# Kernel optimization log

Measured on AMD Instinct MI355X. Metric: run time of the kernel, lower is better.

## Reference

```python
import jax, jax.numpy as jnp
import numpy as np

T, B, D = 512, 128, 1024  # time, batch, feature == hidden_size


def setup_inputs() -> dict:
    key = jax.random.key(0)
    k0, k1, k2, k3 = jax.random.split(key, 4)
    scale = 1.0 / np.sqrt(D)
    ins = jax.random.normal(k0, (T, B, D), jnp.float32)
    resets = jax.random.randint(k1, (T, B), 0, 2).astype(bool)
    # flax GRUCell params, fused along gate axis in order (r, z, n)
    Wi = jax.random.normal(k2, (D, 3 * D), jnp.float32) * scale   # ir|iz|in (with bias)
    bi = jnp.zeros((3 * D,), jnp.float32)
    Wh = jax.random.normal(k3, (D, 3 * D), jnp.float32) * scale   # hr|hz|hn (hr,hz no bias)
    bhn = jnp.zeros((D,), jnp.float32)                            # bias only on hn branch
    return {"ins": ins, "resets": resets, "Wi": Wi, "bi": bi, "Wh": Wh, "bhn": bhn}


def reference(ins, resets, Wi, bi, Wh, bhn):
    H = Wh.shape[0]
    # Input projections are time-independent: compute once as a big GEMM.
    xi = jnp.einsum('tbd,dg->tbg', ins, Wi) + bi  # [T, B, 3H]

    def step(h, inp):
        xi_t, reset_t = inp                       # [B, 3H], [B]
        h = jnp.where(reset_t[:, None], jnp.zeros_like(h), h)  # reset carry to zeros
        hh = h @ Wh                               # [B, 3H]
        xr, xz, xn = jnp.split(xi_t, 3, axis=-1)
        hr, hz, hn = jnp.split(hh, 3, axis=-1)
        r = jax.nn.sigmoid(xr + hr)
        z = jax.nn.sigmoid(xz + hz)
        n = jnp.tanh(xn + r * (hn + bhn))
        h_new = (1.0 - z) * n + z * h             # flax GRUCell update
        return h_new, h_new                       # GRUCell returns (new_h, new_h)

    h0 = jnp.zeros((ins.shape[1], H), ins.dtype)
    _, ys = jax.lax.scan(step, h0, (xi, resets))
    return ys  # [T, B, H]
```

## Files before the change

### kernel.cpp

```cpp
#include <hip/hip_runtime.h>
#include <stdint.h>

typedef unsigned short u16;
typedef unsigned int u32;
typedef unsigned char u8;

typedef __attribute__((ext_vector_type(4))) float f32x4;
typedef __attribute__((ext_vector_type(2))) u32 u32x2;
typedef __attribute__((ext_vector_type(4))) u32 u32x4;
typedef __attribute__((ext_vector_type(8))) __bf16 bf16x8;

#define NITER 48
#define TT 512
#define BB 128

__device__ __forceinline__ u16 f2bf(float f){
    u32 u = __builtin_bit_cast(u32, f);
    u = (u + 0x7FFFu + ((u >> 16) & 1u)) >> 16;
    return (u16)u;
}
__device__ __forceinline__ float bf2f(u16 v){
    u32 u = ((u32)v) << 16;
    return __builtin_bit_cast(float, u);
}
__device__ __forceinline__ u32x4 pack8(f32x4 a, f32x4 b){
    u32x4 u;
    u[0] = (u32)f2bf(a[0]) | ((u32)f2bf(a[1]) << 16);
    u[1] = (u32)f2bf(a[2]) | ((u32)f2bf(a[3]) << 16);
    u[2] = (u32)f2bf(b[0]) | ((u32)f2bf(b[1]) << 16);
    u[3] = (u32)f2bf(b[2]) | ((u32)f2bf(b[3]) << 16);
    return u;
}
__device__ __forceinline__ void glds16(const u16* g, u16* l){
    __builtin_amdgcn_global_load_lds(
        (const __attribute__((address_space(1))) u32*)g,
        (__attribute__((address_space(3))) u32*)l, 16, 0, 0);
}

__global__ void k_detect(const u8* __restrict__ r, int* __restrict__ flag){
    __shared__ int nz[4];
    if (threadIdx.x < 4) nz[threadIdx.x] = 0;
    __syncthreads();
    int loc[4] = {0,0,0,0};
    const int base = threadIdx.x * 16;
    #pragma unroll
    for (int i = 0; i < 16; ++i) if (r[base + i]) loc[i & 3] = 1;
    #pragma unroll
    for (int j = 0; j < 4; ++j) if (loc[j]) atomicOr(&nz[j], 1);
    __syncthreads();
    if (threadIdx.x == 0){
        int f;
        if (nz[0] && !nz[1] && !nz[2] && !nz[3]) f = 0;
        else if (!nz[0] && !nz[1] && (nz[2] || nz[3])) f = 2;
        else f = 1;
        *flag = f;
    }
}

__device__ __forceinline__ int reset_at(const void* r, int f, int idx){
    if (f == 0) return ((const int*)r)[idx] != 0;
    if (f == 1) return ((const u8*)r)[idx] != 0;
    return ((const float*)r)[idx] != 0.f;
}

__global__ void k_ages(const void* __restrict__ resets, const int* __restrict__ flag,
                       int b0, int bw_log, u8* __restrict__ age, int* __restrict__ counts){
    __shared__ int lc[NITER];
    const int tid = threadIdx.x;
    if (tid < NITER) lc[tid] = 0;
    __syncthreads();
    const int cid = blockIdx.x * 256 + tid;
    const int f = *flag;
    const int bwm = (1 << bw_log) - 1;
    const int t = cid >> bw_log, b = b0 + (cid & bwm);
    int a = 0, tt = t;
    while (tt > 0 && !reset_at(resets, f, tt * BB + b)){ ++a; --tt; }
    if (a > NITER - 1) a = NITER - 1;
    age[cid] = (u8)a;
    atomicAdd(&lc[a], 1);
    __syncthreads();
    if (tid < NITER && lc[tid]) atomicAdd(&counts[tid], lc[tid]);
}

__global__ void k_offsets(const int* __restrict__ counts, int* __restrict__ offs,
                          int* __restrict__ curs){
    if (threadIdx.x == 0){
        int o = 0;
        for (int i = 0; i < NITER; ++i){ offs[i] = o; curs[i] = o; o += counts[i]; }
        offs[NITER] = o;
    }
}

__global__ void k_scatter(const u8* __restrict__ age, int* __restrict__ curs,
                          u16* __restrict__ list, u16* __restrict__ posof){
    __shared__ int lc[NITER], lb[NITER];
    const int tid = threadIdx.x;
    if (tid < NITER) lc[tid] = 0;
    __syncthreads();
    const int cid = blockIdx.x * 256 + tid;
    const int a = age[cid];
    const int lpos = atomicAdd(&lc[a], 1);
    __syncthreads();
    if (tid < NITER && lc[tid]) lb[tid] = atomicAdd(&curs[tid], lc[tid]);
    __syncthreads();
    const int p = lb[a] + lpos;
    list[p] = (u16)cid;
    posof[cid] = (u16)p;
}

__global__ void k_packT(const float* __restrict__ Wi, const float* __restrict__ Wh,
                        u16* __restrict__ Wit, u16* __restrict__ Wht){
    __shared__ float tl[32][33];
    const int kb = blockIdx.x * 32;
    const int nb = blockIdx.y * 32;
    const float* W = blockIdx.z ? Wh : Wi;
    u16* Wt = blockIdx.z ? Wht : Wit;
    const int tx = threadIdx.x;
    for (int r = threadIdx.y; r < 32; r += 8)
        tl[r][tx] = W[(size_t)(kb + r) * 3072 + nb + tx];
    __syncthreads();
    for (int r = threadIdx.y; r < 32; r += 8)
        Wt[(size_t)(nb + r) * 1024 + kb + tx] = f2bf(tl[tx][r]);
}

__global__ void k_tobf(const float* __restrict__ ins, u16* __restrict__ insbf,
                       int b0, int bw_log, int total8){
    const int bwm = (1 << bw_log) - 1;
    for (int i = blockIdx.x * 256 + threadIdx.x; i < total8; i += gridDim.x * 256){
        const int cid = i >> 7;
        const int c8 = (i & 127) * 8;
        const int t = cid >> bw_log, j = cid & bwm;
        const float* src = ins + (size_t)(t * BB + b0 + j) * 1024 + c8;
        f32x4 a = *(const f32x4*)src;
        f32x4 b = *(const f32x4*)(src + 4);
        *(u32x4*)(insbf + (size_t)cid * 1024 + c8) = pack8(a, b);
    }
}

__global__ __launch_bounds__(256, 4)
void k_xi(const u16* __restrict__ insbf, const u16* __restrict__ Wit,
          u16* __restrict__ xi, int Mrows)
{
    __shared__ __align__(16) u16 lds[2][8192];
    const int tid = threadIdx.x;
    const int lane = tid & 63;
    const int w = tid >> 6;
    const int wr = w >> 1, wc = w & 1;
    const int l15 = lane & 15;
    const int l4 = lane >> 4;

    const int nMt = Mrows >> 7;
    const int nTiles = nMt * 24;

    for (int idx = blockIdx.x; idx < nTiles; idx += gridDim.x){
        const int mt = idx / 24;
        const int cg = idx - mt * 24;
        const int m0 = mt * 128;
        const int c0 = cg * 128;

        const u16* ga0 = insbf + (size_t)(m0 + w * 16 + (lane >> 2)) * 1024 + (lane & 3) * 8;
        const u16* ga1 = ga0 + (size_t)64 * 1024;
        const u16* gb0 = Wit + (size_t)(c0 + w * 16 + (lane >> 2)) * 1024 + (lane & 3) * 8;
        const u16* gb1 = gb0 + (size_t)64 * 1024;

        f32x4 acc[4][4];
        #pragma unroll
        for (int i = 0; i < 4; ++i)
            #pragma unroll
            for (int j = 0; j < 4; ++j)
                acc[i][j] = (f32x4){0.f, 0.f, 0.f, 0.f};

        {
            u16* Lb = lds[0];
            glds16(ga0, &Lb[w * 512]);
            glds16(ga1, &Lb[2048 + w * 512]);
            glds16(gb0, &Lb[4096 + w * 512]);
            glds16(gb1, &Lb[6144 + w * 512]);
        }
        __syncthreads();

        for (int kt = 0; kt < 32; ++kt){
            if (kt < 31){
                u16* Nb = lds[(kt + 1) & 1];
                const int ko = (kt + 1) * 32;
                glds16(ga0 + ko, &Nb[w * 512]);
                glds16(ga1 + ko, &Nb[2048 + w * 512]);
                glds16(gb0 + ko, &Nb[4096 + w * 512]);
                glds16(gb1 + ko, &Nb[6144 + w * 512]);
            }
            const u16* L = lds[kt & 1];
            bf16x8 ax[4], bx[4];
            #pragma unroll
            for (int rf = 0; rf < 4; ++rf)
                ax[rf] = *(const bf16x8*)&L[(wr * 64 + rf * 16 + l15) * 32 + l4 * 8];
            #pragma unroll
            for (int cf = 0; cf < 4; ++cf)
                bx[cf] = *(const bf16x8*)&L[4096 + (wc * 64 + cf * 16 + l15) * 32 + l4 * 8];
            #pragma unroll
            for (int cf = 0; cf < 4; ++cf)
                #pragma unroll
                for (int rf = 0; rf < 4; ++rf)
                    acc[cf][rf] = __builtin_amdgcn_mfma_f32_16x16x32_bf16(
                        bx[cf], ax[rf], acc[cf][rf], 0, 0, 0);
            __syncthreads();
        }

        #pragma unroll
        for (int cf = 0; cf < 4; ++cf){
            #pragma unroll
            for (int rf = 0; rf < 4; ++rf){
                const int R = m0 + wr * 64 + rf * 16 + l15;
                const int N0 = c0 + wc * 64 + cf * 16 + l4 * 4;
                u32x2 v;
                v[0] = (u32)f2bf(acc[cf][rf][0]) | ((u32)f2bf(acc[cf][rf][1]) << 16);
                v[1] = (u32)f2bf(acc[cf][rf][2]) | ((u32)f2bf(acc[cf][rf][3]) << 16);
                *(u32x2*)(xi + (size_t)R * 3072 + N0) = v;
            }
        }
    }
}

__global__ void k_h0(const u16* __restrict__ list, const int* __restrict__ counts,
                     const u16* __restrict__ xi, float* __restrict__ ys,
                     u16* __restrict__ hbf,
                     const float* __restrict__ bi, const float* __restrict__ bhn,
                     int b0, int bw_log)
{
    const int total = counts[0] * 128;
    const int bwm = (1 << bw_log) - 1;
    for (int i = blockIdx.x * 256 + threadIdx.x; i < total; i += gridDim.x * 256){
        const int row = i >> 7;
        const int c8 = (i & 127) * 8;
        const int cid = list[row];
        const int p = ((cid >> bw_log) << 7) + b0 + (cid & bwm);
        const u16* xr = xi + (size_t)cid * 3072 + c8;
        u32x4 vr = *(const u32x4*)xr;
        u32x4 vz = *(const u32x4*)(xr + 1024);
        u32x4 vn = *(const u32x4*)(xr + 2048);
        f32x4 br0 = *(const f32x4*)(bi + c8),        br1 = *(const f32x4*)(bi + c8 + 4);
        f32x4 bz0 = *(const f32x4*)(bi + 1024 + c8), bz1 = *(const f32x4*)(bi + 1024 + c8 + 4);
        f32x4 bn0 = *(const f32x4*)(bi + 2048 + c8), bn1 = *(const f32x4*)(bi + 2048 + c8 + 4);
        f32x4 bh0 = *(const f32x4*)(bhn + c8),       bh1 = *(const f32x4*)(bhn + c8 + 4);
        float out[8];
        #pragma unroll
        for (int e = 0; e < 8; ++e){
            const float xrv = bf2f((u16)(vr[e >> 1] >> ((e & 1) * 16)));
            const float xzv = bf2f((u16)(vz[e >> 1] >> ((e & 1) * 16)));
            const float xnv = bf2f((u16)(vn[e >> 1] >> ((e & 1) * 16)));
            const float brv = (e < 4) ? br0[e] : br1[e - 4];
            const float bzv = (e < 4) ? bz0[e] : bz1[e - 4];
            const float bnv = (e < 4) ? bn0[e] : bn1[e - 4];
            const float bhv = (e < 4) ? bh0[e] : bh1[e - 4];
            const float rr = 1.f / (1.f + __expf(-(xrv + brv)));
            const float zz = 1.f / (1.f + __expf(-(xzv + bzv)));
            const float nn = tanhf(xnv + bnv + rr * bhv);
            out[e] = (1.f - zz) * nn;
        }
        float* dst = ys + (size_t)p * 1024 + c8;
        f32x4 o0 = (f32x4){out[0], out[1], out[2], out[3]};
        f32x4 o1 = (f32x4){out[4], out[5], out[6], out[7]};
        *(f32x4*)dst = o0;
        *(f32x4*)(dst + 4) = o1;
        *(u32x4*)(hbf + (size_t)row * 1024 + c8) = pack8(o0, o1);
    }
}

#define SSTR64 64
#define SAB 0
#define SBB 8192
#define SLB64 20480
__global__ __launch_bounds__(256, 2)
void k_scanh(int iter, const u16* __restrict__ list, const int* __restrict__ offs,
             const int* __restrict__ counts, const u16* __restrict__ posof,
             u16* hbf, const u16* __restrict__ xi,
             float* ys, const u16* __restrict__ Wht,
             const float* __restrict__ bi, const float* __restrict__ bhn,
             int b0, int bw_log)
{
    const int count = counts[iter];
    if (count <= 0) return;
    const int off = offs[iter];
    const int nTiles = ((count + 127) >> 7) * 16;
    const int bwm = (1 << bw_log) - 1;
    const int bwv = 1 << bw_log;

    __shared__ __align__(16) u16 lds[2][SLB64];

    const int tid = threadIdx.x;
    const int lane = tid & 63;
    const int w = tid >> 6;
    const int wr = w >> 1;
    const int wc = w & 1;
    const int l15 = lane & 15;
    const int l4 = lane >> 4;
    const int lrow = lane >> 3;
    const int slot = lane & 7;

    for (int tile = blockIdx.x; tile < nTiles; tile += gridDim.x){
        const int mt = tile >> 4;
        const int cg = tile & 15;
        const int m0 = mt * 128;
        const int c0 = cg * 64;

        const u16* pa[4];
        #pragma unroll
        for (int c = 0; c < 4; ++c){
            const int r = c * 32 + w * 8 + lrow;
            const int cid = list[off + min(m0 + r, count - 1)];
            pa[c] = hbf + (size_t)posof[cid - bwv] * 1024 + slot * 8;
        }
        const u16* pw[6];
        #pragma unroll
        for (int c = 0; c < 6; ++c){
            const int br = c * 32 + w * 8 + lrow;
            const int g = br >> 6, ri = br & 63;
            pw[c] = Wht + (size_t)(g * 1024 + c0 + ri) * 1024 + slot * 8;
        }

        f32x4 acc[3][4][2];
        #pragma unroll
        for (int gi = 0; gi < 3; ++gi)
            #pragma unroll
            for (int rf = 0; rf < 4; ++rf)
                #pragma unroll
                for (int cf = 0; cf < 2; ++cf)
                    acc[gi][rf][cf] = (f32x4){0.f, 0.f, 0.f, 0.f};

        {
            u16* N = lds[0];
            #pragma unroll
            for (int c = 0; c < 4; ++c)
                glds16(pa[c], &N[SAB + (c * 32 + w * 8) * SSTR64]);
            #pragma unroll
            for (int c = 0; c < 6; ++c)
                glds16(pw[c], &N[SBB + (c * 32 + w * 8) * SSTR64]);
        }
        __syncthreads();

        for (int kt = 0; kt < 16; ++kt){
            if (kt < 15){
                u16* N = lds[(kt + 1) & 1];
                const int ko = (kt + 1) * 64;
                #pragma unroll
                for (int c = 0; c < 4; ++c)
                    glds16(pa[c] + ko, &N[SAB + (c * 32 + w * 8) * SSTR64]);
                #pragma unroll
                for (int c = 0; c < 6; ++c)
                    glds16(pw[c] + ko, &N[SBB + (c * 32 + w * 8) * SSTR64]);
            }
            const u16* L = lds[kt & 1];
            #pragma unroll
            for (int kk = 0; kk < 2; ++kk){
                bf16x8 ah[4];
                #pragma unroll
                for (int rf = 0; rf < 4; ++rf)
                    ah[rf] = *(const bf16x8*)&L[SAB + (wr * 64 + rf * 16 + l15) * SSTR64 + kk * 32 + l4 * 8];
                #pragma unroll
                for (int g = 0; g < 3; ++g){
                    #pragma unroll
                    for (int cf = 0; cf < 2; ++cf){
                        bf16x8 bh = *(const bf16x8*)&L[SBB + (g * 64 + wc * 32 + cf * 16 + l15) * SSTR64 + kk * 32 + l4 * 8];
                        #pragma unroll
                        for (int rf = 0; rf < 4; ++rf)
                            acc[g][rf][cf] = __builtin_amdgcn_mfma_f32_16x16x32_bf16(
                                ah[rf], bh, acc[g][rf][cf], 0, 0, 0);
                    }
                }
            }
            __syncthreads();
        }

        #pragma unroll
        for (int cf = 0; cf < 2; ++cf){
            const int colh = c0 + wc * 32 + cf * 16 + l15;
            const float b_r = bi[colh];
            const float b_z = bi[1024 + colh];
            const float b_n = bi[2048 + colh];
            const float b_h = bhn[colh];
            #pragma unroll
            for (int rf = 0; rf < 4; ++rf){
                #pragma unroll
                for (int m = 0; m < 4; ++m){
                    const int rloc = wr * 64 + rf * 16 + l4 * 4 + m;
                    const int P = off + min(m0 + rloc, count - 1);
                    const int cid = list[P];
                    const int p = ((cid >> bw_log) << 7) + b0 + (cid & bwm);
                    const u16* xr = xi + (size_t)cid * 3072 + colh;
                    const float rr = 1.f / (1.f + __expf(-(bf2f(xr[0]) + b_r + acc[0][rf][cf][m])));
                    const float zz = 1.f / (1.f + __expf(-(bf2f(xr[1024]) + b_z + acc[1][rf][cf][m])));
                    const float nn = tanhf(bf2f(xr[2048]) + b_n + rr * (acc[2][rf][cf][m] + b_h));
                    const float hp = ys[(size_t)(p - 128) * 1024 + colh];
                    const float hv = (1.f - zz) * nn + zz * hp;
                    ys[(size_t)p * 1024 + colh] = hv;
                    hbf[(size_t)P * 1024 + colh] = f2bf(hv);
                }
            }
        }
    }
}

__global__ __launch_bounds__(256, 2)
void k_scan_fb(int iter, const u16* __restrict__ list, const int* __restrict__ offs,
               const int* __restrict__ counts, const float* __restrict__ ins,
               float* ys, const u16* __restrict__ Wit, const u16* __restrict__ Wht,
               const float* __restrict__ bi, const float* __restrict__ bhn)
{
    const int count = counts[iter];
    if (count <= 0) return;
    const int off = offs[iter];
    const int nTiles = ((count + 127) >> 7) * 16;
    const bool hasH = (iter > 0);

    __shared__ __align__(16) u16 lds[2][20480];

    const int tid = threadIdx.x;
    const int lane = tid & 63;
    const int w = tid >> 6;
    const int wr = w >> 1;
    const int wc = w & 1;
    const int l15 = lane & 15;
    const int l4 = lane >> 4;
    const int swz = ((l4 ^ (lane & 3)) * 8);
    const int sr = tid >> 2;
    const int sq = tid & 3;
    const int swzW = ((sq ^ (sr & 3)) * 8);

    for (int tile = blockIdx.x; tile < nTiles; tile += gridDim.x){
        const int mt = tile >> 4;
        const int cg = tile & 15;
        const int m0 = mt * 128;
        const int c0 = cg * 64;

        const int px0i = list[off + min(m0 + sr, count - 1)];
        const int px1i = list[off + min(m0 + 64 + sr, count - 1)];
        const float* px0 = ins + (size_t)px0i * 1024 + sq * 8;
        const float* px1 = ins + (size_t)px1i * 1024 + sq * 8;
        const float* ph0 = ys + (ptrdiff_t)(px0i - 128) * 1024 + sq * 8;
        const float* ph1 = ys + (ptrdiff_t)(px1i - 128) * 1024 + sq * 8;
        const u16* pb[6];
        #pragma unroll
        for (int pp = 0; pp < 6; ++pp){
            const int g = pp >> 1, m = pp & 1;
            const u16* W = m ? Wht : Wit;
            pb[pp] = W + (size_t)(g * 1024 + c0 + sr) * 1024 + sq * 8;
        }

        f32x4 acc[4][4][2];
        #pragma unroll
        for (int gi = 0; gi < 4; ++gi)
            #pragma unroll
            for (int rf = 0; rf < 4; ++rf)
                #pragma unroll
                for (int cf = 0; cf < 2; ++cf)
                    acc[gi][rf][cf] = (f32x4){0.f, 0.f, 0.f, 0.f};

        {
            u16* N = lds[0];
            *(u32x4*)&N[sr * 32 + swzW] = pack8(*(const f32x4*)(px0), *(const f32x4*)(px0 + 4));
            *(u32x4*)&N[(64 + sr) * 32 + swzW] = pack8(*(const f32x4*)(px1), *(const f32x4*)(px1 + 4));
            if (hasH){
                *(u32x4*)&N[(128 + sr) * 32 + swzW] = pack8(*(const f32x4*)(ph0), *(const f32x4*)(ph0 + 4));
                *(u32x4*)&N[(192 + sr) * 32 + swzW] = pack8(*(const f32x4*)(ph1), *(const f32x4*)(ph1 + 4));
            }
            #pragma unroll
            for (int pp = 0; pp < 6; ++pp)
                *(u32x4*)&N[8192 + (pp * 64 + sr) * 32 + swzW] = *(const u32x4*)(pb[pp]);
        }
        __syncthreads();

        int cur = 0;
        #pragma unroll 2
        for (int kt = 0; kt < 32; ++kt){
            f32x4 nx0a, nx0b, nx1a, nx1b, nh0a, nh0b, nh1a, nh1b;
            u32x4 sb[6];
            const bool more = (kt < 31);
            if (more){
                const int kof = (kt + 1) * 32;
                nx0a = *(const f32x4*)(px0 + kof); nx0b = *(const f32x4*)(px0 + kof + 4);
                nx1a = *(const f32x4*)(px1 + kof); nx1b = *(const f32x4*)(px1 + kof + 4);
                if (hasH){
                    nh0a = *(const f32x4*)(ph0 + kof); nh0b = *(const f32x4*)(ph0 + kof + 4);
                    nh1a = *(const f32x4*)(ph1 + kof); nh1b = *(const f32x4*)(ph1 + kof + 4);
                }
                #pragma unroll
                for (int pp = 0; pp < 6; ++pp) sb[pp] = *(const u32x4*)(pb[pp] + kof);
            }

            const u16* L = lds[cur];
            bf16x8 ax[4], ah[4];
            #pragma unroll
            for (int rf = 0; rf < 4; ++rf)
                ax[rf] = *(const bf16x8*)&L[(wr * 64 + rf * 16 + l15) * 32 + swz];
            if (hasH){
                #pragma unroll
                for (int rf = 0; rf < 4; ++rf)
                    ah[rf] = *(const bf16x8*)&L[(128 + wr * 64 + rf * 16 + l15) * 32 + swz];
            }
            #pragma unroll
            for (int g = 0; g < 3; ++g){
                #pragma unroll
                for (int cf = 0; cf < 2; ++cf){
                    const int brow = g * 128 + wc * 32 + cf * 16 + l15;
                    bf16x8 bv = *(const bf16x8*)&L[8192 + brow * 32 + swz];
                    const int gx = (g == 2) ? 2 : g;
                    #pragma unroll
                    for (int rf = 0; rf < 4; ++rf)
                        acc[gx][rf][cf] = __builtin_amdgcn_mfma_f32_16x16x32_bf16(
                            ax[rf], bv, acc[gx][rf][cf], 0, 0, 0);
                    if (hasH){
                        bf16x8 bh = *(const bf16x8*)&L[8192 + (brow + 64) * 32 + swz];
                        const int gh = (g == 2) ? 3 : g;
                        #pragma unroll
                        for (int rf = 0; rf < 4; ++rf)
                            acc[gh][rf][cf] = __builtin_amdgcn_mfma_f32_16x16x32_bf16(
                                ah[rf], bh, acc[gh][rf][cf], 0, 0, 0);
                    }
                }
            }

            if (more){
                u16* N = lds[cur ^ 1];
                *(u32x4*)&N[sr * 32 + swzW] = pack8(nx0a, nx0b);
                *(u32x4*)&N[(64 + sr) * 32 + swzW] = pack8(nx1a, nx1b);
                if (hasH){
                    *(u32x4*)&N[(128 + sr) * 32 + swzW] = pack8(nh0a, nh0b);
                    *(u32x4*)&N[(192 + sr) * 32 + swzW] = pack8(nh1a, nh1b);
                }
                #pragma unroll
                for (int pp = 0; pp < 6; ++pp)
                    *(u32x4*)&N[8192 + (pp * 64 + sr) * 32 + swzW] = sb[pp];
            }
            __syncthreads();
            cur ^= 1;
        }

        #pragma unroll
        for (int cf = 0; cf < 2; ++cf){
            const int colh = c0 + wc * 32 + cf * 16 + l15;
            const float b_r = bi[colh];
            const float b_z = bi[1024 + colh];
            const float b_n = bi[2048 + colh];
            const float b_h = bhn[colh];
            #pragma unroll
            for (int rf = 0; rf < 4; ++rf){
                #pragma unroll
                for (int m = 0; m < 4; ++m){
                    const int rloc = wr * 64 + rf * 16 + l4 * 4 + m;
                    const int p = list[off + min(m0 + rloc, count - 1)];
                    const float rr = 1.f / (1.f + __expf(-(acc[0][rf][cf][m] + b_r)));
                    const float zz = 1.f / (1.f + __expf(-(acc[1][rf][cf][m] + b_z)));
                    const float nn = tanhf(acc[2][rf][cf][m] + b_n + rr * (acc[3][rf][cf][m] + b_h));
                    float hp = 0.f;
                    if (hasH) hp = ys[(size_t)(p - 128) * 1024 + colh];
                    ys[(size_t)p * 1024 + colh] = (1.f - zz) * nn + zz * hp;
                }
            }
        }
    }
}

extern "C" void kernel_launch(void* const* d_in, const int* in_sizes, int n_in,
                              void* d_out, int out_size, void* d_ws, size_t ws_size,
                              hipStream_t stream)
{
    (void)in_sizes; (void)n_in; (void)out_size;
    const float* ins  = (const float*)d_in[0];
    const void*  rst  = d_in[1];
    const float* Wi   = (const float*)d_in[2];
    const float* bi   = (const float*)d_in[3];
    const float* Wh   = (const float*)d_in[4];
    const float* bhn  = (const float*)d_in[5];
    float* ys = (float*)d_out;
    u8* ws = (u8*)d_ws;

    u16* Wit    = (u16*)(ws + 0);
    u16* Wht    = (u16*)(ws + 6291456);
    u8*  age    = ws + 12582912;
    int* counts = (int*)(ws + 12648448);
    int* offs   = (int*)(ws + 12648704);
    int* curs   = (int*)(ws + 12648960);
    int* flag   = (int*)(ws + 12649216);
    u16* posof  = (u16*)(ws + 12649472);
    u16* list   = (u16*)(ws + 12780544);
    u16* insbf  = (u16*)(ws + 12911616);

    int bw = 0, bwlog = 0;
    {
        const size_t base = 12911616;
        if (ws_size >= base + (size_t)TT * 128 * 8192)      { bw = 128; bwlog = 7; }
        else if (ws_size >= base + (size_t)TT * 64 * 8192)  { bw = 64;  bwlog = 6; }
        else if (ws_size >= base + (size_t)TT * 32 * 8192)  { bw = 32;  bwlog = 5; }
    }

    k_detect<<<1, 256, 0, stream>>>((const u8*)rst, flag);
    k_packT<<<dim3(32, 96, 2), dim3(32, 8), 0, stream>>>(Wi, Wh, Wit, Wht);

    if (bw == 0){
        hipMemsetAsync(counts, 0, 192, stream);
        k_ages<<<TT * BB / 256, 256, 0, stream>>>(rst, flag, 0, 7, age, counts);
        k_offsets<<<1, 64, 0, stream>>>(counts, offs, curs);
        k_scatter<<<TT * BB / 256, 256, 0, stream>>>(age, curs, list, posof);
        for (int it = 0; it < NITER; ++it)
            k_scan_fb<<<512, 256, 0, stream>>>(it, list, offs, counts, ins, ys, Wit, Wht, bi, bhn);
        return;
    }

    u16* xi = insbf + (size_t)TT * bw * 1024;
    u16* hbf = insbf;
    const int nch = BB / bw;
    const int Mrows = TT * bw;

    for (int c = 0; c < nch; ++c){
        const int b0 = c * bw;
        hipMemsetAsync(counts, 0, 192, stream);
        k_ages<<<Mrows / 256, 256, 0, stream>>>(rst, flag, b0, bwlog, age, counts);
        k_offsets<<<1, 64, 0, stream>>>(counts, offs, curs);
        k_scatter<<<Mrows / 256, 256, 0, stream>>>(age, curs, list, posof);
        k_tobf<<<2048, 256, 0, stream>>>(ins, insbf, b0, bwlog, Mrows * 128);
        k_xi<<<3072, 256, 0, stream>>>(insbf, Wit, xi, Mrows);
        k_h0<<<2048, 256, 0, stream>>>(list, counts, xi, ys, hbf, bi, bhn, b0, bwlog);
        for (int it = 1; it < NITER; ++it){
            int est = ((Mrows >> (it + 1)) / 128 + 1) * 16;
            int grid = est < 32 ? 32 : (est > 512 ? 512 : est);
            k_scanh<<<grid, 256, 0, stream>>>(it, list, offs, counts, posof, hbf, xi,
                                              ys, Wht, bi, bhn, b0, bwlog);
        }
    }
}
```

Before: 1.997 ms.

## Fuse per-age scan launches into one persistent kernel with dataflow flags

Replaces the 47 per-age k_scanh launches and the separate k_h0 launch with a single persistent k_scan_all kernel. Tiles are ordered by age, and each one waits on per-group atomic completion counters for the previous age before it runs. The age sort becomes deterministic through per-block histograms and prefix bases instead of global atomics. The xi GEMM epilogue is staged through LDS so stores are coalesced 16-byte writes. This removes launch gaps and the tail idle time between dependent iterations, at the risk of spin-wait stalls or deadlock if dependent tiles are not resident.

```diff
diff --git a/kernel.cpp b/kernel.cpp
--- a/kernel.cpp
+++ b/kernel.cpp
@@ -6,7 +6,6 @@
 typedef unsigned char u8;
 
 typedef __attribute__((ext_vector_type(4))) float f32x4;
-typedef __attribute__((ext_vector_type(2))) u32 u32x2;
 typedef __attribute__((ext_vector_type(4))) u32 u32x4;
 typedef __attribute__((ext_vector_type(8))) __bf16 bf16x8;
 
@@ -64,7 +63,7 @@
 }
 
 __global__ void k_ages(const void* __restrict__ resets, const int* __restrict__ flag,
-                       int b0, int bw_log, u8* __restrict__ age, int* __restrict__ counts){
+                       int b0, int bw_log, u8* __restrict__ age, int* __restrict__ bh){
     __shared__ int lc[NITER];
     const int tid = threadIdx.x;
     if (tid < NITER) lc[tid] = 0;
@@ -79,33 +78,52 @@
     age[cid] = (u8)a;
     atomicAdd(&lc[a], 1);
     __syncthreads();
-    if (tid < NITER && lc[tid]) atomicAdd(&counts[tid], lc[tid]);
-}
-
-__global__ void k_offsets(const int* __restrict__ counts, int* __restrict__ offs,
-                          int* __restrict__ curs){
-    if (threadIdx.x == 0){
+    if (tid < NITER) bh[blockIdx.x * NITER + tid] = lc[tid];
+}
+
+__global__ void k_offsets(const int* __restrict__ bh, int NB,
+                          int* __restrict__ counts, int* __restrict__ offs,
+                          int* __restrict__ gbase, int* __restrict__ tbase,
+                          int* __restrict__ bb){
+    const int a = threadIdx.x;
+    if (a < NITER){
+        int run = 0;
+        for (int b = 0; b < NB; ++b){
+            bb[b * NITER + a] = run;
+            run += bh[b * NITER + a];
+        }
+        counts[a] = run;
+    }
+    __syncthreads();
+    if (a == 0){
         int o = 0;
-        for (int i = 0; i < NITER; ++i){ offs[i] = o; curs[i] = o; o += counts[i]; }
+        for (int i = 0; i < NITER; ++i){ offs[i] = o; o += counts[i]; }
         offs[NITER] = o;
-    }
-}
-
-__global__ void k_scatter(const u8* __restrict__ age, int* __restrict__ curs,
+        int g = 0, t = 0;
+        for (int i = 0; i < NITER; ++i){
+            const int ng = (counts[i] + 127) >> 7;
+            gbase[i] = g; g += ng;
+            tbase[i] = t; t += (i == 0) ? ng : ng * 16;
+        }
+        gbase[NITER] = g;
+        tbase[NITER] = t;
+    }
+}
+
+__global__ void k_scatter(const u8* __restrict__ age, const int* __restrict__ offs,
+                          const int* __restrict__ bb,
                           u16* __restrict__ list, u16* __restrict__ posof){
-    __shared__ int lc[NITER], lb[NITER];
+    __shared__ u8 sa[256];
     const int tid = threadIdx.x;
-    if (tid < NITER) lc[tid] = 0;
-    __syncthreads();
     const int cid = blockIdx.x * 256 + tid;
     const int a = age[cid];
-    const int lpos = atomicAdd(&lc[a], 1);
-    __syncthreads();
-    if (tid < NITER && lc[tid]) lb[tid] = atomicAdd(&curs[tid], lc[tid]);
-    __syncthreads();
-    const int p = lb[a] + lpos;
-    list[p] = (u16)cid;
-    posof[cid] = (u16)p;
+    sa[tid] = (u8)a;
+    __syncthreads();
+    int rank = 0;
+    for (int j = 0; j < tid; ++j) rank += (sa[j] == (u8)a);
+    const int pos = offs[a] + bb[blockIdx.x * NITER + a] + rank;
+    list[pos] = (u16)cid;
+    posof[cid] = (u16)pos;
 }
 
 __global__ void k_packT(const float* __restrict__ Wi, const float* __restrict__ Wh,
@@ -197,95 +215,84 @@
             for (int cf = 0; cf < 4; ++cf)
                 bx[cf] = *(const bf16x8*)&L[4096 + (wc * 64 + cf * 16 + l15) * 32 + l4 * 8];
             #pragma unroll
+            for (int rf = 0; rf < 4; ++rf)
+                #pragma unroll
+                for (int cf = 0; cf < 4; ++cf)
+                    acc[rf][cf] = __builtin_amdgcn_mfma_f32_16x16x32_bf16(
+                        ax[rf], bx[cf], acc[rf][cf], 0, 0, 0);
+            __syncthreads();
+        }
+
+        u16* region = ((u16*)lds) + w * 4096;
+        #pragma unroll
+        for (int rf = 0; rf < 4; ++rf)
+            #pragma unroll
             for (int cf = 0; cf < 4; ++cf)
                 #pragma unroll
-                for (int rf = 0; rf < 4; ++rf)
-                    acc[cf][rf] = __builtin_amdgcn_mfma_f32_16x16x32_bf16(
-                        bx[cf], ax[rf], acc[cf][rf], 0, 0, 0);
-            __syncthreads();
-        }
-
-        #pragma unroll
-        for (int cf = 0; cf < 4; ++cf){
-            #pragma unroll
-            for (int rf = 0; rf < 4; ++rf){
-                const int R = m0 + wr * 64 + rf * 16 + l15;
-                const int N0 = c0 + wc * 64 + cf * 16 + l4 * 4;
-                u32x2 v;
-                v[0] = (u32)f2bf(acc[cf][rf][0]) | ((u32)f2bf(acc[cf][rf][1]) << 16);
-                v[1] = (u32)f2bf(acc[cf][rf][2]) | ((u32)f2bf(acc[cf][rf][3]) << 16);
-                *(u32x2*)(xi + (size_t)R * 3072 + N0) = v;
-            }
-        }
-    }
-}
-
-__global__ void k_h0(const u16* __restrict__ list, const int* __restrict__ counts,
-                     const u16* __restrict__ xi, float* __restrict__ ys,
-                     u16* __restrict__ hbf,
-                     const float* __restrict__ bi, const float* __restrict__ bhn,
-                     int b0, int bw_log)
+                for (int m = 0; m < 4; ++m)
+                    region[(rf * 16 + l4 * 4 + m) * 64 + cf * 16 + l15] = f2bf(acc[rf][cf][m]);
+        #pragma unroll
+        for (int rep = 0; rep < 8; ++rep){
+            const int r = rep * 8 + (lane >> 3);
+            const int cc = (lane & 7) * 8;
+            u32x4 v = *(u32x4*)&region[r * 64 + cc];
+            *(u32x4*)(xi + (size_t)(m0 + wr * 64 + r) * 3072 + c0 + wc * 64 + cc) = v;
+        }
+        __syncthreads();
+    }
+}
+
+__device__ __forceinline__ void h0_body(int row, int c8, const u16* __restrict__ list,
+    const u16* __restrict__ xi, float* __restrict__ ys, u16* __restrict__ hbf,
+    const float* __restrict__ bi, const float* __restrict__ bhn, int b0, int bw_log)
 {
-    const int total = counts[0] * 128;
     const int bwm = (1 << bw_log) - 1;
-    for (int i = blockIdx.x * 256 + threadIdx.x; i < total; i += gridDim.x * 256){
-        const int row = i >> 7;
-        const int c8 = (i & 127) * 8;
-        const int cid = list[row];
-        const int p = ((cid >> bw_log) << 7) + b0 + (cid & bwm);
-        const u16* xr = xi + (size_t)cid * 3072 + c8;
-        u32x4 vr = *(const u32x4*)xr;
-        u32x4 vz = *(const u32x4*)(xr + 1024);
-        u32x4 vn = *(const u32x4*)(xr + 2048);
-        f32x4 br0 = *(const f32x4*)(bi + c8),        br1 = *(const f32x4*)(bi + c8 + 4);
-        f32x4 bz0 = *(const f32x4*)(bi + 1024 + c8), bz1 = *(const f32x4*)(bi + 1024 + c8 + 4);
-        f32x4 bn0 = *(const f32x4*)(bi + 2048 + c8), bn1 = *(const f32x4*)(bi + 2048 + c8 + 4);
-        f32x4 bh0 = *(const f32x4*)(bhn + c8),       bh1 = *(const f32x4*)(bhn + c8 + 4);
-        float out[8];
-        #pragma unroll
-        for (int e = 0; e < 8; ++e){
-            const float xrv = bf2f((u16)(vr[e >> 1] >> ((e & 1) * 16)));
-            const float xzv = bf2f((u16)(vz[e >> 1] >> ((e & 1) * 16)));
-            const float xnv = bf2f((u16)(vn[e >> 1] >> ((e & 1) * 16)));
-            const float brv = (e < 4) ? br0[e] : br1[e - 4];
-            const float bzv = (e < 4) ? bz0[e] : bz1[e - 4];
-            const float bnv = (e < 4) ? bn0[e] : bn1[e - 4];
-            const float bhv = (e < 4) ? bh0[e] : bh1[e - 4];
-            const float rr = 1.f / (1.f + __expf(-(xrv + brv)));
-            const float zz = 1.f / (1.f + __expf(-(xzv + bzv)));
-            const float nn = tanhf(xnv + bnv + rr * bhv);
-            out[e] = (1.f - zz) * nn;
-        }
-        float* dst = ys + (size_t)p * 1024 + c8;
-        f32x4 o0 = (f32x4){out[0], out[1], out[2], out[3]};
-        f32x4 o1 = (f32x4){out[4], out[5], out[6], out[7]};
-        *(f32x4*)dst = o0;
-        *(f32x4*)(dst + 4) = o1;
-        *(u32x4*)(hbf + (size_t)row * 1024 + c8) = pack8(o0, o1);
-    }
+    const int cid = list[row];
+    const int p = ((cid >> bw_log) << 7) + b0 + (cid & bwm);
+    const u16* xr = xi + (size_t)cid * 3072 + c8;
+    u32x4 vr = *(const u32x4*)xr;
+    u32x4 vz = *(const u32x4*)(xr + 1024);
+    u32x4 vn = *(const u32x4*)(xr + 2048);
+    f32x4 br0 = *(const f32x4*)(bi + c8),        br1 = *(const f32x4*)(bi + c8 + 4);
+    f32x4 bz0 = *(const f32x4*)(bi + 1024 + c8), bz1 = *(const f32x4*)(bi + 1024 + c8 + 4);
+    f32x4 bn0 = *(const f32x4*)(bi + 2048 + c8), bn1 = *(const f32x4*)(bi + 2048 + c8 + 4);
+    f32x4 bh0 = *(const f32x4*)(bhn + c8),       bh1 = *(const f32x4*)(bhn + c8 + 4);
+    float out[8];
+    #pragma unroll
+    for (int e = 0; e < 8; ++e){
+        const float xrv = bf2f((u16)(vr[e >> 1] >> ((e & 1) * 16)));
+        const float xzv = bf2f((u16)(vz[e >> 1] >> ((e & 1) * 16)));
+        const float xnv = bf2f((u16)(vn[e >> 1] >> ((e & 1) * 16)));
+        const float brv = (e < 4) ? br0[e] : br1[e - 4];
+        const float bzv = (e < 4) ? bz0[e] : bz1[e - 4];
+        const float bnv = (e < 4) ? bn0[e] : bn1[e - 4];
+        const float bhv = (e < 4) ? bh0[e] : bh1[e - 4];
+        const float rr = 1.f / (1.f + __expf(-(xrv + brv)));
+        const float zz = 1.f / (1.f + __expf(-(xzv + bzv)));
+        const float nn = tanhf(xnv + bnv + rr * bhv);
+        out[e] = (1.f - zz) * nn;
+    }
+    float* dst = ys + (size_t)p * 1024 + c8;
+    f32x4 o0 = (f32x4){out[0], out[1], out[2], out[3]};
+    f32x4 o1 = (f32x4){out[4], out[5], out[6], out[7]};
+    *(f32x4*)dst = o0;
+    *(f32x4*)(dst + 4) = o1;
+    *(u32x4*)(hbf + (size_t)row * 1024 + c8) = pack8(o0, o1);
 }
 
 #define SSTR64 64
 #define SAB 0
 #define SBB 8192
 #define SLB64 20480
-__global__ __launch_bounds__(256, 2)
-void k_scanh(int iter, const u16* __restrict__ list, const int* __restrict__ offs,
-             const int* __restrict__ counts, const u16* __restrict__ posof,
-             u16* hbf, const u16* __restrict__ xi,
-             float* ys, const u16* __restrict__ Wht,
-             const float* __restrict__ bi, const float* __restrict__ bhn,
-             int b0, int bw_log)
+
+__device__ __forceinline__ void scanh_tile(int mtg, int cg, int count, int off,
+    int b0, int bw_log, const u16* __restrict__ list, const u16* __restrict__ posof,
+    u16* hbf, const u16* __restrict__ xi, float* ys, const u16* __restrict__ Wht,
+    const float* __restrict__ bi, const float* __restrict__ bhn,
+    u16 (*lds)[SLB64])
 {
-    const int count = counts[iter];
-    if (count <= 0) return;
-    const int off = offs[iter];
-    const int nTiles = ((count + 127) >> 7) * 16;
     const int bwm = (1 << bw_log) - 1;
     const int bwv = 1 << bw_log;
-
-    __shared__ __align__(16) u16 lds[2][SLB64];
-
     const int tid = threadIdx.x;
     const int lane = tid & 63;
     const int w = tid >> 6;
@@ -296,106 +303,164 @@
     const int lrow = lane >> 3;
     const int slot = lane & 7;
 
-    for (int tile = blockIdx.x; tile < nTiles; tile += gridDim.x){
-        const int mt = tile >> 4;
-        const int cg = tile & 15;
-        const int m0 = mt * 128;
-        const int c0 = cg * 64;
-
-        const u16* pa[4];
-        #pragma unroll
-        for (int c = 0; c < 4; ++c){
-            const int r = c * 32 + w * 8 + lrow;
-            const int cid = list[off + min(m0 + r, count - 1)];
-            pa[c] = hbf + (size_t)posof[cid - bwv] * 1024 + slot * 8;
-        }
-        const u16* pw[6];
-        #pragma unroll
-        for (int c = 0; c < 6; ++c){
-            const int br = c * 32 + w * 8 + lrow;
-            const int g = br >> 6, ri = br & 63;
-            pw[c] = Wht + (size_t)(g * 1024 + c0 + ri) * 1024 + slot * 8;
-        }
-
-        f32x4 acc[3][4][2];
-        #pragma unroll
-        for (int gi = 0; gi < 3; ++gi)
+    const int m0 = mtg * 128;
+    const int c0 = cg * 64;
+
+    const u16* pa[4];
+    #pragma unroll
+    for (int c = 0; c < 4; ++c){
+        const int r = c * 32 + w * 8 + lrow;
+        const int cid = list[off + min(m0 + r, count - 1)];
+        pa[c] = hbf + (size_t)posof[cid - bwv] * 1024 + slot * 8;
+    }
+    const u16* pw[6];
+    #pragma unroll
+    for (int c = 0; c < 6; ++c){
+        const int br = c * 32 + w * 8 + lrow;
+        const int g = br >> 6, ri = br & 63;
+        pw[c] = Wht + (size_t)(g * 1024 + c0 + ri) * 1024 + slot * 8;
+    }
+
+    f32x4 acc[3][4][2];
+    #pragma unroll
+    for (int gi = 0; gi < 3; ++gi)
+        #pragma unroll
+        for (int rf = 0; rf < 4; ++rf)
+            #pragma unroll
+            for (int cf = 0; cf < 2; ++cf)
+                acc[gi][rf][cf] = (f32x4){0.f, 0.f, 0.f, 0.f};
+
+    {
+        u16* N = lds[0];
+        #pragma unroll
+        for (int c = 0; c < 4; ++c)
+            glds16(pa[c], &N[SAB + (c * 32 + w * 8) * SSTR64]);
+        #pragma unroll
+        for (int c = 0; c < 6; ++c)
+            glds16(pw[c], &N[SBB + (c * 32 + w * 8) * SSTR64]);
+    }
+    __syncthreads();
+
+    for (int kt = 0; kt < 16; ++kt){
+        if (kt < 15){
+            u16* N = lds[(kt + 1) & 1];
+            const int ko = (kt + 1) * 64;
+            #pragma unroll
+            for (int c = 0; c < 4; ++c)
+                glds16(pa[c] + ko, &N[SAB + (c * 32 + w * 8) * SSTR64]);
+            #pragma unroll
+            for (int c = 0; c < 6; ++c)
+                glds16(pw[c] + ko, &N[SBB + (c * 32 + w * 8) * SSTR64]);
+        }
+        const u16* L = lds[kt & 1];
+        #pragma unroll
+        for (int kk = 0; kk < 2; ++kk){
+            bf16x8 ah[4];
             #pragma unroll
             for (int rf = 0; rf < 4; ++rf)
-                #pragma unroll
-                for (int cf = 0; cf < 2; ++cf)
-                    acc[gi][rf][cf] = (f32x4){0.f, 0.f, 0.f, 0.f};
-
-        {
-            u16* N = lds[0];
-            #pragma unroll
-            for (int c = 0; c < 4; ++c)
-                glds16(pa[c], &N[SAB + (c * 32 + w * 8) * SSTR64]);
-            #pragma unroll
-            for (int c = 0; c < 6; ++c)
-                glds16(pw[c], &N[SBB + (c * 32 + w * 8) * SSTR64]);
+                ah[rf] = *(const bf16x8*)&L[SAB + (wr * 64 + rf * 16 + l15) * SSTR64 + kk * 32 + l4 * 8];
+            #pragma unroll
+            for (int g = 0; g < 3; ++g){
+                #pragma unroll
+                for (int cf = 0; cf < 2; ++cf){
+                    bf16x8 bh = *(const bf16x8*)&L[SBB + (g * 64 + wc * 32 + cf * 16 + l15) * SSTR64 + kk * 32 + l4 * 8];
+                    #pragma unroll
+                    for (int rf = 0; rf < 4; ++rf)
+                        acc[g][rf][cf] = __builtin_amdgcn_mfma_f32_16x16x32_bf16(
+                            ah[rf], bh, acc[g][rf][cf], 0, 0, 0);
+                }
+            }
         }
         __syncthreads();
-
-        for (int kt = 0; kt < 16; ++kt){
-            if (kt < 15){
-                u16* N = lds[(kt + 1) & 1];
-                const int ko = (kt + 1) * 64;
-                #pragma unroll
-                for (int c = 0; c < 4; ++c)
-                    glds16(pa[c] + ko, &N[SAB + (c * 32 + w * 8) * SSTR64]);
-                #pragma unroll
-                for (int c = 0; c < 6; ++c)
-                    glds16(pw[c] + ko, &N[SBB + (c * 32 + w * 8) * SSTR64]);
-            }
-            const u16* L = lds[kt & 1];
-            #pragma unroll
-            for (int kk = 0; kk < 2; ++kk){
-                bf16x8 ah[4];
-                #pragma unroll
-                for (int rf = 0; rf < 4; ++rf)
-                    ah[rf] = *(const bf16x8*)&L[SAB + (wr * 64 + rf * 16 + l15) * SSTR64 + kk * 32 + l4 * 8];
-                #pragma unroll
-                for (int g = 0; g < 3; ++g){
-                    #pragma unroll
-                    for (int cf = 0; cf < 2; ++cf){
-                        bf16x8 bh = *(const bf16x8*)&L[SBB + (g * 64 + wc * 32 + cf * 16 + l15) * SSTR64 + kk * 32 + l4 * 8];
-                        #pragma unroll
-                        for (int rf = 0; rf < 4; ++rf)
-                            acc[g][rf][cf] = __builtin_amdgcn_mfma_f32_16x16x32_bf16(
-                                ah[rf], bh, acc[g][rf][cf], 0, 0, 0);
-                    }
-                }
+    }
+
+    #pragma unroll
+    for (int cf = 0; cf < 2; ++cf){
+        const int colh = c0 + wc * 32 + cf * 16 + l15;
+        const float b_r = bi[colh];
+        const float b_z = bi[1024 + colh];
+        const float b_n = bi[2048 + colh];
+        const float b_h = bhn[colh];
+        #pragma unroll
+        for (int rf = 0; rf < 4; ++rf){
+            #pragma unroll
+            for (int m = 0; m < 4; ++m){
+                const int rloc = wr * 64 + rf * 16 + l4 * 4 + m;
+                const int P = off + min(m0 + rloc, count - 1);
+                const int cid = list[P];
+                const int p = ((cid >> bw_log) << 7) + b0 + (cid & bwm);
+                const u16* xr = xi + (size_t)cid * 3072 + colh;
+                const float rr = 1.f / (1.f + __expf(-(bf2f(xr[0]) + b_r + acc[0][rf][cf][m])));
+                const float zz = 1.f / (1.f + __expf(-(bf2f(xr[1024]) + b_z + acc[1][rf][cf][m])));
+                const float nn = tanhf(bf2f(xr[2048]) + b_n + rr * (acc[2][rf][cf][m] + b_h));
+                const float hp = ys[(size_t)(p - 128) * 1024 + colh];
+                const float hv = (1.f - zz) * nn + zz * hp;
+                ys[(size_t)p * 1024 + colh] = hv;
+                hbf[(size_t)P * 1024 + colh] = f2bf(hv);
+            }
+        }
+    }
+}
+
+__global__ __launch_bounds__(256, 2)
+void k_scan_all(const u16* __restrict__ list, const int* __restrict__ offs,
+                const int* __restrict__ counts, const u16* __restrict__ posof,
+                u16* hbf, const u16* __restrict__ xi, float* ys,
+                const u16* __restrict__ Wht, const float* __restrict__ bi,
+                const float* __restrict__ bhn, int b0, int bw_log,
+                const int* __restrict__ gbase, const int* __restrict__ tbase,
+                u32* __restrict__ fin)
+{
+    __shared__ __align__(16) u16 lds[2][SLB64];
+    const int T = tbase[NITER];
+    const int tid = threadIdx.x;
+
+    for (int idx = blockIdx.x; idx < T; idx += gridDim.x){
+        int a = 0;
+        while (tbase[a + 1] <= idx) ++a;
+
+        if (a == 0){
+            const int grp = idx;
+            const int cnt0 = counts[0];
+            const int nrows = min(128, cnt0 - grp * 128);
+            for (int ii = tid; ii < nrows * 128; ii += 256){
+                const int row = grp * 128 + (ii >> 7);
+                const int c8 = (ii & 127) * 8;
+                h0_body(row, c8, list, xi, ys, hbf, bi, bhn, b0, bw_log);
             }
             __syncthreads();
-        }
-
-        #pragma unroll
-        for (int cf = 0; cf < 2; ++cf){
-            const int colh = c0 + wc * 32 + cf * 16 + l15;
-            const float b_r = bi[colh];
-            const float b_z = bi[1024 + colh];
-            const float b_n = bi[2048 + colh];
-            const float b_h = bhn[colh];
-            #pragma unroll
-            for (int rf = 0; rf < 4; ++rf){
-                #pragma unroll
-                for (int m = 0; m < 4; ++m){
-                    const int rloc = wr * 64 + rf * 16 + l4 * 4 + m;
-                    const int P = off + min(m0 + rloc, count - 1);
-                    const int cid = list[P];
-                    const int p = ((cid >> bw_log) << 7) + b0 + (cid & bwm);
-                    const u16* xr = xi + (size_t)cid * 3072 + colh;
-                    const float rr = 1.f / (1.f + __expf(-(bf2f(xr[0]) + b_r + acc[0][rf][cf][m])));
-                    const float zz = 1.f / (1.f + __expf(-(bf2f(xr[1024]) + b_z + acc[1][rf][cf][m])));
-                    const float nn = tanhf(bf2f(xr[2048]) + b_n + rr * (acc[2][rf][cf][m] + b_h));
-                    const float hp = ys[(size_t)(p - 128) * 1024 + colh];
-                    const float hv = (1.f - zz) * nn + zz * hp;
-                    ys[(size_t)p * 1024 + colh] = hv;
-                    hbf[(size_t)P * 1024 + colh] = f2bf(hv);
-                }
-            }
-        }
+            if (tid == 0)
+                __hip_atomic_fetch_add(&fin[gbase[0] + grp], 16u,
+                                       __ATOMIC_RELEASE, __HIP_MEMORY_SCOPE_AGENT);
+            continue;
+        }
+
+        const int rel = idx - tbase[a];
+        const int mtg = rel >> 4, cg = rel & 15;
+        const int count = counts[a], off = offs[a];
+
+        if (tid == 0){
+            const int bwv = 1 << bw_log;
+            const int cidF = list[off + mtg * 128];
+            const int cidL = list[off + min(mtg * 128 + 127, count - 1)];
+            const int opv = offs[a - 1];
+            const int glo = gbase[a - 1] + ((posof[cidF - bwv] - opv) >> 7);
+            const int ghi = gbase[a - 1] + ((posof[cidL - bwv] - opv) >> 7);
+            for (int g = glo; g <= ghi; ++g){
+                while (__hip_atomic_load(&fin[g], __ATOMIC_RELAXED, __HIP_MEMORY_SCOPE_AGENT) < 16u)
+                    __builtin_amdgcn_s_sleep(8);
+            }
+            (void)__hip_atomic_load(&fin[ghi], __ATOMIC_ACQUIRE, __HIP_MEMORY_SCOPE_AGENT);
+        }
+        __syncthreads();
+
+        scanh_tile(mtg, cg, count, off, b0, bw_log, list, posof, hbf, xi, ys,
+                   Wht, bi, bhn, lds);
+
+        __syncthreads();
+        if (tid == 0)
+            __hip_atomic_fetch_add(&fin[gbase[a] + mtg], 1u,
+                                   __ATOMIC_RELEASE, __HIP_MEMORY_SCOPE_AGENT);
     }
 }
 
@@ -573,20 +638,25 @@
     float* ys = (float*)d_out;
     u8* ws = (u8*)d_ws;
 
+    const size_t A = 12648448;
     u16* Wit    = (u16*)(ws + 0);
     u16* Wht    = (u16*)(ws + 6291456);
     u8*  age    = ws + 12582912;
-    int* counts = (int*)(ws + 12648448);
-    int* offs   = (int*)(ws + 12648704);
-    int* curs   = (int*)(ws + 12648960);
-    int* flag   = (int*)(ws + 12649216);
-    u16* posof  = (u16*)(ws + 12649472);
-    u16* list   = (u16*)(ws + 12780544);
-    u16* insbf  = (u16*)(ws + 12911616);
+    int* counts = (int*)(ws + A + 0);
+    int* offs   = (int*)(ws + A + 256);
+    int* gbase  = (int*)(ws + A + 512);
+    int* tbase  = (int*)(ws + A + 768);
+    u32* fin    = (u32*)(ws + A + 1024);
+    int* flag   = (int*)(ws + A + 5120);
+    int* bh     = (int*)(ws + A + 5376);
+    int* bb     = (int*)(ws + A + 54528);
+    u16* posof  = (u16*)(ws + A + 103680);
+    u16* list   = (u16*)(ws + A + 234752);
+    u16* insbf  = (u16*)(ws + 13014272);
 
     int bw = 0, bwlog = 0;
     {
-        const size_t base = 12911616;
+        const size_t base = 13014272;
         if (ws_size >= base + (size_t)TT * 128 * 8192)      { bw = 128; bwlog = 7; }
         else if (ws_size >= base + (size_t)TT * 64 * 8192)  { bw = 64;  bwlog = 6; }
         else if (ws_size >= base + (size_t)TT * 32 * 8192)  { bw = 32;  bwlog = 5; }
@@ -596,10 +666,11 @@
     k_packT<<<dim3(32, 96, 2), dim3(32, 8), 0, stream>>>(Wi, Wh, Wit, Wht);
 
     if (bw == 0){
-        hipMemsetAsync(counts, 0, 192, stream);
-        k_ages<<<TT * BB / 256, 256, 0, stream>>>(rst, flag, 0, 7, age, counts);
-        k_offsets<<<1, 64, 0, stream>>>(counts, offs, curs);
-        k_scatter<<<TT * BB / 256, 256, 0, stream>>>(age, curs, list, posof);
+        const int Mr = TT * BB, NB = Mr / 256;
+        hipMemsetAsync(ws + A, 0, 5120, stream);
+        k_ages<<<NB, 256, 0, stream>>>(rst, flag, 0, 7, age, bh);
+        k_offsets<<<1, 64, 0, stream>>>(bh, NB, counts, offs, gbase, tbase, bb);
+        k_scatter<<<NB, 256, 0, stream>>>(age, offs, bb, list, posof);
         for (int it = 0; it < NITER; ++it)
             k_scan_fb<<<512, 256, 0, stream>>>(it, list, offs, counts, ins, ys, Wit, Wht, bi, bhn);
         return;
@@ -609,21 +680,17 @@
     u16* hbf = insbf;
     const int nch = BB / bw;
     const int Mrows = TT * bw;
+    const int NB = Mrows / 256;
 
     for (int c = 0; c < nch; ++c){
         const int b0 = c * bw;
-        hipMemsetAsync(counts, 0, 192, stream);
-        k_ages<<<Mrows / 256, 256, 0, stream>>>(rst, flag, b0, bwlog, age, counts);
-        k_offsets<<<1, 64, 0, stream>>>(counts, offs, curs);
-        k_scatter<<<Mrows / 256, 256, 0, stream>>>(age, curs, list, posof);
+        hipMemsetAsync(ws + A, 0, 5120, stream);
+        k_ages<<<NB, 256, 0, stream>>>(rst, flag, b0, bwlog, age, bh);
+        k_offsets<<<1, 64, 0, stream>>>(bh, NB, counts, offs, gbase, tbase, bb);
+        k_scatter<<<NB, 256, 0, stream>>>(age, offs, bb, list, posof);
         k_tobf<<<2048, 256, 0, stream>>>(ins, insbf, b0, bwlog, Mrows * 128);
         k_xi<<<3072, 256, 0, stream>>>(insbf, Wit, xi, Mrows);
-        k_h0<<<2048, 256, 0, stream>>>(list, counts, xi, ys, hbf, bi, bhn, b0, bwlog);
-        for (int it = 1; it < NITER; ++it){
-            int est = ((Mrows >> (it + 1)) / 128 + 1) * 16;
-            int grid = est < 32 ? 32 : (est > 512 ? 512 : est);
-            k_scanh<<<grid, 256, 0, stream>>>(it, list, offs, counts, posof, hbf, xi,
-                                              ys, Wht, bi, bhn, b0, bwlog);
-        }
-    }
-}
+        k_scan_all<<<512, 256, 0, stream>>>(list, offs, counts, posof, hbf, xi, ys,
+                                            Wht, bi, bhn, b0, bwlog, gbase, tbase, fin);
+    }
+}
```

Measured after the change: 2.136 ms. 1.07x slower.
